# Optimization experiments

Measured on AMD Instinct MI355X. Metric: run time of the kernel, lower is better.

## Reference

```python
import jax, jax.numpy as jnp
import numpy as np

BITS = 8
EPS = 1e-5
NUM_HEADS = 16


def ste_round(x):
    # straight-through rounding (matches brevitas round STE)
    return x + jax.lax.stop_gradient(jnp.round(x) - x)


def _scale(stat, qmax):
    return jnp.maximum(stat, 1e-8) / qmax


def fq_act_signed(x, bits=BITS):
    # runtime max-abs per-tensor scale (approximates brevitas runtime percentile 99.999)
    qmax = 2 ** (bits - 1) - 1
    qmin = -(2 ** (bits - 1))
    s = _scale(jnp.max(jnp.abs(x)), qmax)
    return jnp.clip(ste_round(x / s), qmin, qmax) * s


def fq_act_unsigned(x, bits=BITS):
    qmax = 2 ** bits - 1
    s = _scale(jnp.max(x), qmax)
    return jnp.clip(ste_round(x / s), 0, qmax) * s


def fq_weight(w, bits=BITS):
    # NarrowIntQuant + MaxStatsScaling: symmetric narrow range [-qmax, qmax]
    qmax = 2 ** (bits - 1) - 1
    s = _scale(jnp.max(jnp.abs(w)), qmax)
    return jnp.clip(ste_round(w / s), -qmax, qmax) * s


def fq_bias(b, bits=BITS):
    qmax = 2 ** (bits - 1) - 1
    qmin = -(2 ** (bits - 1))
    s = _scale(jnp.max(jnp.abs(b)), qmax)
    return jnp.clip(ste_round(b / s), qmin, qmax) * s


def layernorm(x):
    # elementwise_affine=False
    m = jnp.mean(x, axis=-1, keepdims=True)
    v = jnp.mean((x - m) ** 2, axis=-1, keepdims=True)
    return (x - m) / jnp.sqrt(v + EPS)


def setup_inputs() -> dict:
    key = jax.random.key(0)
    ks = jax.random.split(key, 13)
    B, S, E, M = 4, 1024, 1024, 4096
    std = 0.02
    inp = {
        "x": jax.random.normal(ks[0], (B, S, E), jnp.float32),
        "Wq": jax.random.normal(ks[1], (E, E), jnp.float32) * std,
        "bq": jax.random.normal(ks[2], (E,), jnp.float32) * std,
        "Wk": jax.random.normal(ks[3], (E, E), jnp.float32) * std,
        "bk": jax.random.normal(ks[4], (E,), jnp.float32) * std,
        "Wv": jax.random.normal(ks[5], (E, E), jnp.float32) * std,
        "bv": jax.random.normal(ks[6], (E,), jnp.float32) * std,
        "Wo": jax.random.normal(ks[7], (E, E), jnp.float32) * std,
        "bo": jax.random.normal(ks[8], (E,), jnp.float32) * std,
        "W1": jax.random.normal(ks[9], (M, E), jnp.float32) * std,
        "b1": jax.random.normal(ks[10], (M,), jnp.float32) * std,
        "W2": jax.random.normal(ks[11], (E, M), jnp.float32) * std,
        "b2": jax.random.normal(ks[12], (E,), jnp.float32) * std,
    }
    return inp


def reference(x, Wq, bq, Wk, bk, Wv, bv, Wo, bo, W1, b1, W2, b2):
    B, S, E = x.shape
    H = NUM_HEADS
    D = E // H
    # causal additive mask [S, S]
    i = jnp.arange(S)
    mask = jnp.where(i[None, :] <= i[:, None], 0.0, -jnp.inf).astype(x.dtype)

    # sdp_input_quant (shared q=k=v input)
    q_in = fq_act_signed(x)

    # quantized in-proj (packed_in_proj=False -> separate q/k/v projections)
    Q = q_in @ fq_weight(Wq).T + fq_bias(bq)
    K = q_in @ fq_weight(Wk).T + fq_bias(bk)
    V = q_in @ fq_weight(Wv).T + fq_bias(bv)

    Qh = Q.reshape(B, S, H, D)
    Kh = K.reshape(B, S, H, D)
    Vh = V.reshape(B, S, H, D)

    qs = fq_act_signed(Qh / jnp.sqrt(jnp.asarray(D, x.dtype)))  # q_scaled_quant
    kq = fq_act_signed(Kh)  # k_transposed_quant (per-tensor -> transpose-invariant)
    vq = fq_act_signed(Vh)  # v_quant

    scores = jnp.einsum("bqhd,bkhd->bhqk", qs, kq) + mask  # [B,H,S,S]
    attn = fq_act_signed(jax.nn.softmax(scores, axis=-1))  # attn_output_weights_quant

    ctx = jnp.einsum("bhqk,bkhd->bqhd", attn, vq).reshape(B, S, E)
    ctx = fq_act_signed(ctx)  # out_proj_input_quant
    attn_out = ctx @ fq_weight(Wo).T + fq_bias(bo)

    # residual_sdp: QuantEltwiseAdd quantizes both inputs, then layer-norm
    x1 = layernorm(fq_act_signed(x) + fq_act_signed(attn_out))

    # MLP: QuantIdentity -> QuantLinear -> QuantReLU -> QuantLinear
    h = fq_act_signed(x1) @ fq_weight(W1).T + fq_bias(b1)
    h = fq_act_unsigned(jax.nn.relu(h))
    h = h @ fq_weight(W2).T + fq_bias(b2)

    out = layernorm(fq_act_signed(x1) + fq_act_signed(h))
    return out
```

## Files before the change

kernel.cpp:

```cpp
#include <hip/hip_runtime.h>
#include <stdint.h>
#include <stddef.h>


typedef unsigned short u16;
typedef __attribute__((ext_vector_type(4))) int   i32x4;
typedef __attribute__((ext_vector_type(4))) float f32x4;

#define DEV __device__ __forceinline__

DEV float bf2f(u16 u) { return __uint_as_float(((unsigned)u) << 16); }
DEV void atomicMaxF(float* p, float v) { atomicMax((unsigned*)p, __float_as_uint(v)); }
DEV float waveMax(float v) {
#pragma unroll
  for (int o = 32; o; o >>= 1) v = fmaxf(v, __shfl_xor(v, o, 64));
  return v;
}
DEV float waveSum(float v) {
#pragma unroll
  for (int o = 32; o; o >>= 1) v += __shfl_xor(v, o, 64);
  return v;
}
DEV int waveSumI(int v) {
#pragma unroll
  for (int o = 32; o; o >>= 1) v += __shfl_xor(v, o, 64);
  return v;
}
DEV void blockStatMax(float v, float* __restrict__ slot64, float* sred4, int flatBlk) {
  v = waveMax(v);
  const int tid = threadIdx.x;
  if ((tid & 63) == 0) sred4[tid >> 6] = v;
  __syncthreads();
  if (tid == 0) {
    float m = fmaxf(fmaxf(sred4[0], sred4[1]), fmaxf(sred4[2], sred4[3]));
    atomicMaxF(&slot64[flatBlk & 63], m);
  }
}
DEV float slotMax64(const float* __restrict__ s) {
  float m = 0.f;
#pragma unroll
  for (int i = 0; i < 64; ++i) m = fmaxf(m, s[i]);
  return m;
}
DEV f32x4 ld4(const void* p, int i4, int isf32) {
  if (isf32) return ((const f32x4*)p)[i4];
  ushort4 u = ((const ushort4*)p)[i4];
  return (f32x4){bf2f(u.x), bf2f(u.y), bf2f(u.z), bf2f(u.w)};
}
DEV void gll16(const void* g, void* l) {
  __builtin_amdgcn_global_load_lds((__attribute__((address_space(1))) void*)(g),
                                   (__attribute__((address_space(3))) void*)(l),
                                   16, 0, 0);
}
DEV unsigned ldsaddr(const void* p) {
  return (unsigned)(size_t)(__attribute__((address_space(3))) const void*)p;
}
DEV unsigned quadsel(unsigned a, unsigned b, unsigned c, unsigned d, int idx) {
  unsigned lo = (idx & 1) ? b : a;
  unsigned hi = (idx & 1) ? d : c;
  return (idx & 2) ? hi : lo;
}

__global__ void detect_f32(const u16* __restrict__ x, int* __restrict__ flag) {
  const int tid = threadIdx.x;
  int cnt = 0;
#pragma unroll
  for (int i = 0; i < 16; ++i) {
    u16 u = x[tid * 16 + i];
    if ((u & 0x7f80u) >= 0x4380u) ++cnt;
  }
  cnt = waveSumI(cnt);
  if (tid == 0) flag[0] = (cnt > 16) ? 1 : 0;
}

struct AJobs { const void* p[13]; int n4[13]; int bstart[14]; };

__global__ __launch_bounds__(256) void absmax_multi(AJobs J, float* __restrict__ M,
                                                    const int* __restrict__ flagp) {
  __shared__ float sred[4];
  const int isf32 = flagp[0];
  const int blk = blockIdx.x, tid = threadIdx.x;
  int j = 0;
  while (j < 12 && blk >= J.bstart[j + 1]) ++j;
  const int lb = blk - J.bstart[j];
  const int nb = J.bstart[j + 1] - J.bstart[j];
  float mx = 0.f;
  const void* p = J.p[j];
  for (int i = lb * 256 + tid; i < J.n4[j]; i += nb * 256) {
    f32x4 v = ld4(p, i, isf32);
    mx = fmaxf(mx, fmaxf(fmaxf(fabsf(v.x), fabsf(v.y)),
                         fmaxf(fabsf(v.z), fabsf(v.w))));
  }
  blockStatMax(mx, M + j * 64, sred, lb);
}

__global__ __launch_bounds__(256) void quant_in_signed(
    const void* __restrict__ in, int8_t* __restrict__ out,
    const float* __restrict__ mp, const int* __restrict__ flagp, int n4) {
  const int isf32 = flagp[0];
  const float s = fmaxf(slotMax64(mp), 1e-8f) / 127.0f;
  char4* op = (char4*)out;
  for (int i = blockIdx.x * 256 + threadIdx.x; i < n4; i += gridDim.x * 256) {
    f32x4 v = ld4(in, i, isf32);
    char4 q;
    q.x = (signed char)fminf(fmaxf(rintf(v.x / s), -128.f), 127.f);
    q.y = (signed char)fminf(fmaxf(rintf(v.y / s), -128.f), 127.f);
    q.z = (signed char)fminf(fmaxf(rintf(v.z / s), -128.f), 127.f);
    q.w = (signed char)fminf(fmaxf(rintf(v.w / s), -128.f), 127.f);
    op[i] = q;
  }
}

struct WJobs { const void* in[5]; int8_t* out[5]; int mslot[5]; int n4[5]; int bstart[6]; };

__global__ __launch_bounds__(256) void quant_w_multi(WJobs J, const float* __restrict__ M,
                                                     const int* __restrict__ flagp) {
  const int isf32 = flagp[0];
  const int blk = blockIdx.x, tid = threadIdx.x;
  int j = 0;
  while (j < 4 && blk >= J.bstart[j + 1]) ++j;
  const int lb = blk - J.bstart[j];
  const int nb = J.bstart[j + 1] - J.bstart[j];
  const float s = fmaxf(slotMax64(M + J.mslot[j] * 64), 1e-8f) / 127.0f;
  const void* p = J.in[j];
  char4* o = (char4*)J.out[j];
  for (int i = lb * 256 + tid; i < J.n4[j]; i += nb * 256) {
    f32x4 v = ld4(p, i, isf32);
    char4 q;
    q.x = (signed char)fminf(fmaxf(rintf(v.x / s), -127.f), 127.f);
    q.y = (signed char)fminf(fmaxf(rintf(v.y / s), -127.f), 127.f);
    q.z = (signed char)fminf(fmaxf(rintf(v.z / s), -127.f), 127.f);
    q.w = (signed char)fminf(fmaxf(rintf(v.w / s), -127.f), 127.f);
    o[i] = q;
  }
}

__global__ __launch_bounds__(256) void quant_w2_rs(
    const void* __restrict__ w2, int8_t* __restrict__ out,
    const float* __restrict__ mp, const int* __restrict__ flagp,
    int* __restrict__ rowsum) {
  const int isf32 = flagp[0];
  const int row = blockIdx.x, tid = threadIdx.x;
  const float s = fmaxf(slotMax64(mp), 1e-8f) / 127.0f;
  char4* op = (char4*)(out + (size_t)row * 4096);
  int sum = 0;
  for (int i = tid; i < 1024; i += 256) {
    f32x4 v = ld4(w2, row * 1024 + i, isf32);
    char4 q;
    q.x = (signed char)fminf(fmaxf(rintf(v.x / s), -127.f), 127.f);
    q.y = (signed char)fminf(fmaxf(rintf(v.y / s), -127.f), 127.f);
    q.z = (signed char)fminf(fmaxf(rintf(v.z / s), -127.f), 127.f);
    q.w = (signed char)fminf(fmaxf(rintf(v.w / s), -127.f), 127.f);
    op[i] = q;
    sum += (int)q.x + (int)q.y + (int)q.z + (int)q.w;
  }
  sum = waveSumI(sum);
  __shared__ int rs4[4];
  if ((tid & 63) == 0) rs4[tid >> 6] = sum;
  __syncthreads();
  if (tid == 0) rowsum[row] = rs4[0] + rs4[1] + rs4[2] + rs4[3];
}

struct BJobs { const void* in[6]; float* out[6]; int mslot[6]; int n4[6]; };

__global__ __launch_bounds__(256) void fq_bias_multi(BJobs J, const float* __restrict__ M,
                                                     const int* __restrict__ flagp) {
  const int isf32 = flagp[0];
  const int j = blockIdx.x;
  const float s = fmaxf(slotMax64(M + J.mslot[j] * 64), 1e-8f) / 127.0f;
  float* o = J.out[j];
  for (int i = threadIdx.x; i < J.n4[j]; i += 256) {
    f32x4 v = ld4(J.in[j], i, isf32);
    f32x4 r;
    r.x = fminf(fmaxf(rintf(v.x / s), -128.f), 127.f) * s;
    r.y = fminf(fmaxf(rintf(v.y / s), -128.f), 127.f) * s;
    r.z = fminf(fmaxf(rintf(v.z / s), -128.f), 127.f) * s;
    r.w = fminf(fmaxf(rintf(v.w / s), -128.f), 127.f) * s;
    *(f32x4*)(o + i * 4) = r;
  }
}

__global__ __launch_bounds__(256) void quant_f32_signed(
    const float* __restrict__ in, int8_t* __restrict__ out,
    const float* __restrict__ mp, float pre, int n4) {
  const float s = fmaxf(slotMax64(mp) * pre, 1e-8f) / 127.0f;
  const f32x4* ip = (const f32x4*)in;
  char4* op = (char4*)out;
  for (int i = blockIdx.x * 256 + threadIdx.x; i < n4; i += gridDim.x * 256) {
    f32x4 v = ip[i];
    char4 q;
    q.x = (signed char)fminf(fmaxf(rintf(v.x * pre / s), -128.f), 127.f);
    q.y = (signed char)fminf(fmaxf(rintf(v.y * pre / s), -128.f), 127.f);
    q.z = (signed char)fminf(fmaxf(rintf(v.z * pre / s), -128.f), 127.f);
    q.w = (signed char)fminf(fmaxf(rintf(v.w * pre / s), -128.f), 127.f);
    op[i] = q;
  }
}

__global__ __launch_bounds__(256) void quant_v_t(
    const float* __restrict__ V, int8_t* __restrict__ Vt,
    const float* __restrict__ mp) {
  __shared__ float tile[64][65];
  const int bh = blockIdx.x, st = blockIdx.y;
  const int b = bh >> 4, h = bh & 15;
  const int tid = threadIdx.x;
  const float s = fmaxf(slotMax64(mp), 1e-8f) / 127.0f;
  const int r = tid >> 2, c = (tid & 3) * 16;
  const float* src = V + ((size_t)(b * 1024 + st * 64 + r)) * 1024 + h * 64 + c;
#pragma unroll
  for (int g = 0; g < 4; ++g) {
    f32x4 v = *(const f32x4*)(src + g * 4);
    tile[r][c + g * 4 + 0] = v.x;
    tile[r][c + g * 4 + 1] = v.y;
    tile[r][c + g * 4 + 2] = v.z;
    tile[r][c + g * 4 + 3] = v.w;
  }
  __syncthreads();
  unsigned wds[4];
#pragma unroll
  for (int g = 0; g < 4; ++g) {
    unsigned wd = 0;
#pragma unroll
    for (int k = 0; k < 4; ++k) {
      float v = tile[c + g * 4 + k][r];
      int q = (int)fminf(fmaxf(rintf(v / s), -128.f), 127.f);
      wd |= ((unsigned)(unsigned char)(signed char)q) << (8 * k);
    }
    wds[g] = wd;
  }
  i32x4 ov = {(int)wds[0], (int)wds[1], (int)wds[2], (int)wds[3]};
  *(i32x4*)(Vt + ((size_t)((b * 16 + h) * 64 + r)) * 1024 + st * 64 + c) = ov;
}

__global__ __launch_bounds__(256) void gemm_i8(
    const int8_t* __restrict__ A, const int8_t* __restrict__ B,
    float* __restrict__ Cf, int8_t* __restrict__ Cq,
    const float* __restrict__ mA, float preA, float qmaxA,
    const float* __restrict__ mB,
    const float* __restrict__ bias, const int* __restrict__ extra,
    int relu, int mode, float* __restrict__ mOut, int K, int O) {
  __shared__ __align__(16) int8_t smem[4][12288];
  __shared__ float sred[4];
  const int tid = threadIdx.x;
  const int nb = blockIdx.x, ob = blockIdx.y;
  const int w = tid >> 6, lane = tid & 63, l15 = lane & 15, quad = lane >> 4;
  i32x4 acc[2][4];
#pragma unroll
  for (int i = 0; i < 2; ++i)
#pragma unroll
    for (int j = 0; j < 4; ++j) acc[i][j] = (i32x4){0, 0, 0, 0};
  const int r0 = tid >> 2, c0 = (tid & 3) * 16;
  const int8_t* Ab = A + (size_t)(nb * 128) * K;
  const int8_t* Bb = B + (size_t)(ob * 64) * K;
  const int nk = K >> 6;
  const int aoffl = (w * 32 + l15) * 64 + quad * 16;
  const int boffl = 8192 + l15 * 64 + quad * 16;
  for (int t = 0; t < 3 && t < nk; ++t) {
    const size_t kt0 = (size_t)t << 6;
    int8_t* d = smem[t];
    gll16(Ab + (size_t)r0 * K + kt0 + c0, d + tid * 16);
    gll16(Ab + (size_t)(r0 + 64) * K + kt0 + c0, d + 4096 + tid * 16);
    gll16(Bb + (size_t)r0 * K + kt0 + c0, d + 8192 + tid * 16);
  }
  for (int i = 0; i < nk; ++i) {
    const int infl = nk - 1 - i;
    if (infl >= 2)      asm volatile("s_waitcnt vmcnt(6)" ::: "memory");
    else if (infl == 1) asm volatile("s_waitcnt vmcnt(3)" ::: "memory");
    else                asm volatile("s_waitcnt vmcnt(0)" ::: "memory");
    asm volatile("s_barrier" ::: "memory");
    if (i + 3 < nk) {
      const size_t kt0 = (size_t)(i + 3) << 6;
      int8_t* d = smem[(i + 3) & 3];
      gll16(Ab + (size_t)r0 * K + kt0 + c0, d + tid * 16);
      gll16(Ab + (size_t)(r0 + 64) * K + kt0 + c0, d + 4096 + tid * 16);
      gll16(Bb + (size_t)r0 * K + kt0 + c0, d + 8192 + tid * 16);
    }
    const unsigned a_addr = ldsaddr(smem[i & 3] + aoffl);
    const unsigned b_addr = ldsaddr(smem[i & 3] + boffl);
    i32x4 af[2], bf[4];
    asm volatile("ds_read_b128 %0, %1 offset:0"    : "=v"(af[0]) : "v"(a_addr));
    asm volatile("ds_read_b128 %0, %1 offset:1024" : "=v"(af[1]) : "v"(a_addr));
    asm volatile("ds_read_b128 %0, %1 offset:0"    : "=v"(bf[0]) : "v"(b_addr));
    asm volatile("ds_read_b128 %0, %1 offset:1024" : "=v"(bf[1]) : "v"(b_addr));
    asm volatile("ds_read_b128 %0, %1 offset:2048" : "=v"(bf[2]) : "v"(b_addr));
    asm volatile("ds_read_b128 %0, %1 offset:3072" : "=v"(bf[3]) : "v"(b_addr));
    asm volatile("s_waitcnt lgkmcnt(0)" ::: "memory");
    __builtin_amdgcn_sched_barrier(0);
#pragma unroll
    for (int mt = 0; mt < 2; ++mt)
#pragma unroll
      for (int nt = 0; nt < 4; ++nt)
        acc[mt][nt] = __builtin_amdgcn_mfma_i32_16x16x64_i8(af[mt], bf[nt], acc[mt][nt], 0, 0, 0);
  }
  const float sA = fmaxf(slotMax64(mA) * preA, 1e-8f) / qmaxA;
  const float sB = fmaxf(slotMax64(mB), 1e-8f) / 127.0f;
  const float sAB = sA * sB;
  const float sq = (mode == 2) ? (fmaxf(slotMax64(mOut), 1e-8f) / 255.0f) : 1.0f;
  float lmax = 0.f;
#pragma unroll
  for (int mt = 0; mt < 2; ++mt) {
    const int n = nb * 128 + w * 32 + mt * 16 + quad * 4;
#pragma unroll
    for (int nt = 0; nt < 4; ++nt) {
      const int o = ob * 64 + nt * 16 + l15;
      const int ext = extra ? 128 * extra[o] : 0;
      const float bv = bias[o];
#pragma unroll
      for (int r = 0; r < 4; ++r) {
        float v = sAB * (float)(acc[mt][nt][r] + ext) + bv;
        if (relu) v = fmaxf(v, 0.f);
        if (mode == 0) Cf[(size_t)(n + r) * O + o] = v;
        else if (mode == 2) {
          int q = (int)fminf(fmaxf(rintf(v / sq), 0.f), 255.f) - 128;
          Cq[(size_t)(n + r) * O + o] = (int8_t)q;
        }
        lmax = fmaxf(lmax, fabsf(v));
      }
    }
  }
  if (mode != 2)
    blockStatMax(lmax, mOut, sred, nb + ob * gridDim.x);
}

__global__ __launch_bounds__(256, 4) void attn_fused(
    const int8_t* __restrict__ Qq, const int8_t* __restrict__ Kq,
    const int8_t* __restrict__ Vt, float* __restrict__ ctx,
    const float* __restrict__ M, float* __restrict__ mOut) {
  __shared__ __align__(16) int8_t qtile[4096];
  __shared__ __align__(16) int8_t ktile[4][4096];
  __shared__ __align__(16) int8_t vtile[4][4096];
  __shared__ float sred[4];
  const int tid = threadIdx.x, bid = blockIdx.x;
  const int pidx = bid & 7, rh = (bid >> 3) & 1, h = (bid >> 4) & 15, b = bid >> 8;
  const int qthi = 15 - pidx, qtlo = pidx, ktmax = qthi;
  const int w = tid >> 6, lane = tid & 63, l15 = lane & 15, quad = lane >> 4;
  const int wqt = (w < 2) ? qthi : qtlo;
  const int wrow0 = rh * 32 + (w & 1) * 16;
  const float sqs = fmaxf(slotMax64(M + 13 * 64) * 0.125f, 1e-8f) / 127.0f;
  const float sk = fmaxf(slotMax64(M + 14 * 64), 1e-8f) / 127.0f;
  const float sv = fmaxf(slotMax64(M + 15 * 64), 1e-8f) / 127.0f;
  const float sqk = sqs * sk;
  const float s_attn = 1.0f / 127.0f;
  const int r0 = tid >> 2, c0 = (tid & 3) * 16;
  const int8_t* Kbase = Kq + (size_t)(b * 1024) * 1024 + h * 64 + c0;
  const int8_t* Vbase = Vt + (size_t)((b * 16 + h) * 64 + r0) * 1024 + c0;
  const unsigned fragoff = (unsigned)(l15 * 64 + quad * 16);

  {
    const int qt_s = (r0 < 32) ? qthi : qtlo;
    const int qrow_g = qt_s * 64 + rh * 32 + (r0 & 31);
    gll16(Qq + ((size_t)(b * 1024 + qrow_g)) * 1024 + h * 64 + c0, qtile + tid * 16);
  }
#pragma unroll
  for (int t = 0; t < 3; ++t)
    gll16(Kbase + (size_t)(t * 64 + r0) * 1024, ktile[t] + tid * 16);
  asm volatile("s_waitcnt vmcnt(3)" ::: "memory");
  asm volatile("s_barrier" ::: "memory");
  i32x4 aq;
  {
    const unsigned qa = ldsaddr(qtile) + (unsigned)((w * 16 + l15) * 64 + quad * 16);
    asm volatile("ds_read_b128 %0, %1 offset:0" : "=v"(aq) : "v"(qa));
    asm volatile("s_waitcnt lgkmcnt(0)" ::: "memory");
  }
  const int qrow = wqt * 64 + wrow0 + l15;

  float m_l = -1e30f, l_l = 0.f;
  for (int kt = 0; kt <= ktmax; ++kt) {
    if (kt + 2 <= ktmax)      asm volatile("s_waitcnt vmcnt(2)" ::: "memory");
    else if (kt + 1 <= ktmax) asm volatile("s_waitcnt vmcnt(1)" ::: "memory");
    else                      asm volatile("s_waitcnt vmcnt(0)" ::: "memory");
    asm volatile("s_barrier" ::: "memory");
    if (kt + 3 <= ktmax)
      gll16(Kbase + (size_t)((kt + 3) * 64 + r0) * 1024, ktile[(kt + 3) & 3] + tid * 16);
    if (kt <= wqt) {
      const unsigned ka = ldsaddr(ktile[kt & 3]) + fragoff;
      i32x4 bk[4];
      asm volatile("ds_read_b128 %0, %1 offset:0"    : "=v"(bk[0]) : "v"(ka));
      asm volatile("ds_read_b128 %0, %1 offset:1024" : "=v"(bk[1]) : "v"(ka));
      asm volatile("ds_read_b128 %0, %1 offset:2048" : "=v"(bk[2]) : "v"(ka));
      asm volatile("ds_read_b128 %0, %1 offset:3072" : "=v"(bk[3]) : "v"(ka));
      asm volatile("s_waitcnt lgkmcnt(0)" ::: "memory");
      __builtin_amdgcn_sched_barrier(0);
      const int kc0 = kt * 64 + quad * 4;
      float sc[4][4];
#pragma unroll
      for (int nt = 0; nt < 4; ++nt) {
        i32x4 z = {0, 0, 0, 0};
        i32x4 d = __builtin_amdgcn_mfma_i32_16x16x64_i8(bk[nt], aq, z, 0, 0, 0);
        if (kt == wqt) {
#pragma unroll
          for (int r = 0; r < 4; ++r)
            sc[nt][r] = (kc0 + nt * 16 + r <= qrow) ? sqk * (float)d[r] : -1e30f;
        } else {
#pragma unroll
          for (int r = 0; r < 4; ++r) sc[nt][r] = sqk * (float)d[r];
        }
      }
      float vm = sc[0][0];
#pragma unroll
      for (int nt = 0; nt < 4; ++nt)
#pragma unroll
        for (int r = 0; r < 4; ++r) vm = fmaxf(vm, sc[nt][r]);
      const float mn = fmaxf(m_l, vm);
      float sum = 0.f;
#pragma unroll
      for (int nt = 0; nt < 4; ++nt)
#pragma unroll
        for (int r = 0; r < 4; ++r) sum += __expf(sc[nt][r] - mn);
      l_l = l_l * __expf(m_l - mn) + sum;
      m_l = mn;
    }
  }
#pragma unroll
  for (int off = 16; off <= 32; off <<= 1) {
    float om = __shfl_xor(m_l, off, 64);
    float ol = __shfl_xor(l_l, off, 64);
    float mn = fmaxf(m_l, om);
    l_l = l_l * __expf(m_l - mn) + ol * __expf(om - mn);
    m_l = mn;
  }
  const float rl127 = 127.0f / l_l;

  __syncthreads();
#pragma unroll
  for (int t = 0; t < 3; ++t) {
    gll16(Kbase + (size_t)(t * 64 + r0) * 1024, ktile[t] + tid * 16);
    gll16(Vbase + t * 64, vtile[t] + tid * 16);
  }
  i32x4 cacc[4] = {{0, 0, 0, 0}, {0, 0, 0, 0}, {0, 0, 0, 0}, {0, 0, 0, 0}};
  for (int kt = 0; kt <= ktmax; ++kt) {
    if (kt + 2 <= ktmax)      asm volatile("s_waitcnt vmcnt(4)" ::: "memory");
    else if (kt + 1 <= ktmax) asm volatile("s_waitcnt vmcnt(2)" ::: "memory");
    else                      asm volatile("s_waitcnt vmcnt(0)" ::: "memory");
    asm volatile("s_barrier" ::: "memory");
    if (kt + 3 <= ktmax) {
      gll16(Kbase + (size_t)((kt + 3) * 64 + r0) * 1024, ktile[(kt + 3) & 3] + tid * 16);
      gll16(Vbase + (kt + 3) * 64, vtile[(kt + 3) & 3] + tid * 16);
    }
    if (kt <= wqt) {
      const unsigned ka = ldsaddr(ktile[kt & 3]) + fragoff;
      const unsigned va = ldsaddr(vtile[kt & 3]) + fragoff;
      i32x4 bk[4], bv[4];
      asm volatile("ds_read_b128 %0, %1 offset:0"    : "=v"(bk[0]) : "v"(ka));
      asm volatile("ds_read_b128 %0, %1 offset:1024" : "=v"(bk[1]) : "v"(ka));
      asm volatile("ds_read_b128 %0, %1 offset:2048" : "=v"(bk[2]) : "v"(ka));
      asm volatile("ds_read_b128 %0, %1 offset:3072" : "=v"(bk[3]) : "v"(ka));
      asm volatile("ds_read_b128 %0, %1 offset:0"    : "=v"(bv[0]) : "v"(va));
      asm volatile("ds_read_b128 %0, %1 offset:1024" : "=v"(bv[1]) : "v"(va));
      asm volatile("ds_read_b128 %0, %1 offset:2048" : "=v"(bv[2]) : "v"(va));
      asm volatile("ds_read_b128 %0, %1 offset:3072" : "=v"(bv[3]) : "v"(va));
      asm volatile("s_waitcnt lgkmcnt(0)" ::: "memory");
      __builtin_amdgcn_sched_barrier(0);
      const int kc0 = kt * 64 + quad * 4;
      unsigned Dw[4];
#pragma unroll
      for (int nt = 0; nt < 4; ++nt) {
        i32x4 z = {0, 0, 0, 0};
        i32x4 d = __builtin_amdgcn_mfma_i32_16x16x64_i8(bk[nt], aq, z, 0, 0, 0);
        unsigned wd = 0;
        if (kt == wqt) {
#pragma unroll
          for (int r = 0; r < 4; ++r) {
            float e = (kc0 + nt * 16 + r <= qrow)
                          ? __expf(sqk * (float)d[r] - m_l) * rl127 : 0.f;
            wd |= ((unsigned)(int)rintf(e)) << (8 * r);
          }
        } else {
#pragma unroll
          for (int r = 0; r < 4; ++r) {
            float e = __expf(sqk * (float)d[r] - m_l) * rl127;
            wd |= ((unsigned)(int)rintf(e)) << (8 * r);
          }
        }
        Dw[nt] = wd;
      }
      unsigned selfv = quadsel(Dw[0], Dw[1], Dw[2], Dw[3], quad);
      unsigned rv1 = (unsigned)__shfl_xor(
          (int)quadsel(Dw[0], Dw[1], Dw[2], Dw[3], quad ^ 1), 16, 64);
      unsigned rv2 = (unsigned)__shfl_xor(
          (int)quadsel(Dw[0], Dw[1], Dw[2], Dw[3], quad ^ 2), 32, 64);
      unsigned rv3 = (unsigned)__shfl_xor(
          (int)quadsel(Dw[0], Dw[1], Dw[2], Dw[3], quad ^ 3), 48, 64);
      i32x4 pf;
#pragma unroll
      for (int j = 0; j < 4; ++j) {
        const int t = j ^ quad;
        pf[j] = (int)((t == 0) ? selfv : (t == 1) ? rv1 : (t == 2) ? rv2 : rv3);
      }
#pragma unroll
      for (int nt = 0; nt < 4; ++nt)
        cacc[nt] = __builtin_amdgcn_mfma_i32_16x16x64_i8(pf, bv[nt], cacc[nt], 0, 0, 0);
    }
  }
  const float sc2 = s_attn * sv;
  float lmax = 0.f;
  const int orow0 = wqt * 64 + wrow0 + quad * 4;
#pragma unroll
  for (int nt = 0; nt < 4; ++nt) {
    const int d = nt * 16 + l15;
#pragma unroll
    for (int r = 0; r < 4; ++r) {
      float v = sc2 * (float)cacc[nt][r];
      ctx[((size_t)(b * 1024 + orow0 + r)) * 1024 + h * 64 + d] = v;
      lmax = fmaxf(lmax, fabsf(v));
    }
  }
  blockStatMax(lmax, mOut, sred, bid);
}

__global__ __launch_bounds__(256) void ln_res(
    const int8_t* __restrict__ xq, const float* __restrict__ mx,
    const float* __restrict__ ao, const float* __restrict__ ma,
    float* __restrict__ x1, float* __restrict__ mOut) {
  __shared__ float red[8];
  __shared__ float sred[4];
  const int row = blockIdx.x, tid = threadIdx.x;
  const float sx = fmaxf(slotMax64(mx), 1e-8f) / 127.0f;
  const float sa = fmaxf(slotMax64(ma), 1e-8f) / 127.0f;
  char4 xv = *(const char4*)(xq + (size_t)row * 1024 + tid * 4);
  f32x4 av = *(const f32x4*)(ao + (size_t)row * 1024 + tid * 4);
  float t[4];
  t[0] = (float)xv.x * sx + fminf(fmaxf(rintf(av.x / sa), -128.f), 127.f) * sa;
  t[1] = (float)xv.y * sx + fminf(fmaxf(rintf(av.y / sa), -128.f), 127.f) * sa;
  t[2] = (float)xv.z * sx + fminf(fmaxf(rintf(av.z / sa), -128.f), 127.f) * sa;
  t[3] = (float)xv.w * sx + fminf(fmaxf(rintf(av.w / sa), -128.f), 127.f) * sa;
  float s = waveSum(t[0] + t[1] + t[2] + t[3]);
  if ((tid & 63) == 0) red[tid >> 6] = s;
  __syncthreads();
  const float mean = (red[0] + red[1] + red[2] + red[3]) * (1.0f / 1024.0f);
  float vs = 0.f;
#pragma unroll
  for (int i = 0; i < 4; ++i) { float d = t[i] - mean; vs += d * d; }
  vs = waveSum(vs);
  if ((tid & 63) == 0) red[4 + (tid >> 6)] = vs;
  __syncthreads();
  const float var = (red[4] + red[5] + red[6] + red[7]) * (1.0f / 1024.0f);
  const float rs = sqrtf(var + 1e-5f);
  f32x4 o;
  o.x = (t[0] - mean) / rs;
  o.y = (t[1] - mean) / rs;
  o.z = (t[2] - mean) / rs;
  o.w = (t[3] - mean) / rs;
  *(f32x4*)(x1 + (size_t)row * 1024 + tid * 4) = o;
  float lmax = fmaxf(fmaxf(fabsf(o.x), fabsf(o.y)), fmaxf(fabsf(o.z), fabsf(o.w)));
  blockStatMax(lmax, mOut, sred, row);
}

__global__ __launch_bounds__(256) void ln_final(
    const int8_t* __restrict__ x1q, const float* __restrict__ mx1,
    const float* __restrict__ h2, const float* __restrict__ mh2,
    float* __restrict__ out) {
  __shared__ float red[8];
  const int row = blockIdx.x, tid = threadIdx.x;
  const float s1 = fmaxf(slotMax64(mx1), 1e-8f) / 127.0f;
  const float s2 = fmaxf(slotMax64(mh2), 1e-8f) / 127.0f;
  char4 xv = *(const char4*)(x1q + (size_t)row * 1024 + tid * 4);
  f32x4 hv = *(const f32x4*)(h2 + (size_t)row * 1024 + tid * 4);
  float t[4];
  t[0] = (float)xv.x * s1 + fminf(fmaxf(rintf(hv.x / s2), -128.f), 127.f) * s2;
  t[1] = (float)xv.y * s1 + fminf(fmaxf(rintf(hv.y / s2), -128.f), 127.f) * s2;
  t[2] = (float)xv.z * s1 + fminf(fmaxf(rintf(hv.z / s2), -128.f), 127.f) * s2;
  t[3] = (float)xv.w * s1 + fminf(fmaxf(rintf(hv.w / s2), -128.f), 127.f) * s2;
  float s = waveSum(t[0] + t[1] + t[2] + t[3]);
  if ((tid & 63) == 0) red[tid >> 6] = s;
  __syncthreads();
  const float mean = (red[0] + red[1] + red[2] + red[3]) * (1.0f / 1024.0f);
  float vs = 0.f;
#pragma unroll
  for (int i = 0; i < 4; ++i) { float d = t[i] - mean; vs += d * d; }
  vs = waveSum(vs);
  if ((tid & 63) == 0) red[4 + (tid >> 6)] = vs;
  __syncthreads();
  const float var = (red[4] + red[5] + red[6] + red[7]) * (1.0f / 1024.0f);
  const float rs = sqrtf(var + 1e-5f);
  f32x4 o;
  o.x = (t[0] - mean) / rs;
  o.y = (t[1] - mean) / rs;
  o.z = (t[2] - mean) / rs;
  o.w = (t[3] - mean) / rs;
  *(f32x4*)(out + (size_t)row * 1024 + tid * 4) = o;
}

static constexpr size_t MB = 1u << 20;
static constexpr size_t OFF_M     = 0;
static constexpr size_t OFF_FLAG  = 6400;
static constexpr size_t OFF_BIASQ = 8192;
static constexpr size_t OFF_BIASK = OFF_BIASQ + 4096;
static constexpr size_t OFF_BIASV = OFF_BIASK + 4096;
static constexpr size_t OFF_BIASO = OFF_BIASV + 4096;
static constexpr size_t OFF_BIAS1 = OFF_BIASO + 4096;
static constexpr size_t OFF_BIAS2 = OFF_BIAS1 + 16384;
static constexpr size_t OFF_RS    = OFF_BIAS2 + 4096;
static constexpr size_t OFF_XQ    = 65536;
static constexpr size_t OFF_WQQ   = OFF_XQ  + 4 * MB;
static constexpr size_t OFF_WKQ   = OFF_WQQ + 1 * MB;
static constexpr size_t OFF_WVQ   = OFF_WKQ + 1 * MB;
static constexpr size_t OFF_WOQ   = OFF_WVQ + 1 * MB;
static constexpr size_t OFF_W1Q   = OFF_WOQ + 1 * MB;
static constexpr size_t OFF_W2Q   = OFF_W1Q + 4 * MB;
static constexpr size_t OFF_X1Q   = OFF_W2Q + 4 * MB;
static constexpr size_t OFF_A1    = OFF_X1Q + 4 * MB;
static constexpr size_t OFF_A2    = OFF_A1 + 16 * MB;

extern "C" void kernel_launch(void* const* d_in, const int* in_sizes, int n_in,
                              void* d_out, int out_size, void* d_ws, size_t ws_size,
                              hipStream_t stream) {
  (void)n_in; (void)out_size; (void)ws_size;
  char* ws = (char*)d_ws;
  float* M = (float*)(ws + OFF_M);
  int* FLAG = (int*)(ws + OFF_FLAG);
  float* BIASQ = (float*)(ws + OFF_BIASQ);
  float* BIASK = (float*)(ws + OFF_BIASK);
  float* BIASV = (float*)(ws + OFF_BIASV);
  float* BIASO = (float*)(ws + OFF_BIASO);
  float* BIAS1 = (float*)(ws + OFF_BIAS1);
  float* BIAS2 = (float*)(ws + OFF_BIAS2);
  int* RS = (int*)(ws + OFF_RS);
  int8_t* XQ  = (int8_t*)(ws + OFF_XQ);
  int8_t* WQQ = (int8_t*)(ws + OFF_WQQ);
  int8_t* WKQ = (int8_t*)(ws + OFF_WKQ);
  int8_t* WVQ = (int8_t*)(ws + OFF_WVQ);
  int8_t* WOQ = (int8_t*)(ws + OFF_WOQ);
  int8_t* W1Q = (int8_t*)(ws + OFF_W1Q);
  int8_t* W2Q = (int8_t*)(ws + OFF_W2Q);
  int8_t* X1Q = (int8_t*)(ws + OFF_X1Q);
  int8_t* QQ   = (int8_t*)(ws + OFF_A1);
  int8_t* KQQ  = (int8_t*)(ws + OFF_A1 + 4 * MB);
  int8_t* VT   = (int8_t*)(ws + OFF_A1 + 8 * MB);
  int8_t* CTXQ = (int8_t*)(ws + OFF_A1 + 12 * MB);
  float*  X1F  = (float*)(ws + OFF_A1);
  int8_t* HQ   = (int8_t*)(ws + OFF_A1);
  float* FBUF = (float*)(ws + OFF_A2);

  hipMemsetAsync(M, 0, 8192, stream);
  detect_f32<<<1, 64, 0, stream>>>((const u16*)d_in[0], FLAG);

  AJobs aj;
  const int ablk[13] = {512, 128, 1, 128, 1, 128, 1, 128, 1, 512, 2, 512, 1};
  int bs = 0;
  for (int i = 0; i < 13; ++i) {
    aj.p[i] = d_in[i];
    aj.n4[i] = in_sizes[i] / 4;
    aj.bstart[i] = bs;
    bs += ablk[i];
  }
  aj.bstart[13] = bs;
  absmax_multi<<<bs, 256, 0, stream>>>(aj, M, FLAG);

  quant_in_signed<<<1024, 256, 0, stream>>>(d_in[0], XQ, M + 0 * 64, FLAG, in_sizes[0] / 4);

  WJobs wj;
  const int widx[5] = {1, 3, 5, 7, 9};
  int8_t* wout[5] = {WQQ, WKQ, WVQ, WOQ, W1Q};
  const int wblk[5] = {128, 128, 128, 128, 512};
  int wb = 0;
  for (int j = 0; j < 5; ++j) {
    wj.in[j] = d_in[widx[j]];
    wj.out[j] = wout[j];
    wj.mslot[j] = widx[j];
    wj.n4[j] = in_sizes[widx[j]] / 4;
    wj.bstart[j] = wb;
    wb += wblk[j];
  }
  wj.bstart[5] = wb;
  quant_w_multi<<<wb, 256, 0, stream>>>(wj, M, FLAG);
  quant_w2_rs<<<1024, 256, 0, stream>>>(d_in[11], W2Q, M + 11 * 64, FLAG, RS);

  BJobs bj;
  const int bidx[6] = {2, 4, 6, 8, 10, 12};
  float* bout[6] = {BIASQ, BIASK, BIASV, BIASO, BIAS1, BIAS2};
  for (int j = 0; j < 6; ++j) {
    bj.in[j] = d_in[bidx[j]];
    bj.out[j] = bout[j];
    bj.mslot[j] = bidx[j];
    bj.n4[j] = in_sizes[bidx[j]] / 4;
  }
  fq_bias_multi<<<6, 256, 0, stream>>>(bj, M, FLAG);

  gemm_i8<<<dim3(32, 16), 256, 0, stream>>>(XQ, WQQ, FBUF, nullptr, M + 0 * 64, 1.f, 127.f, M + 1 * 64, BIASQ, nullptr, 0, 0, M + 13 * 64, 1024, 1024);
  quant_f32_signed<<<2048, 256, 0, stream>>>(FBUF, QQ, M + 13 * 64, 0.125f, 1024 * 1024);
  gemm_i8<<<dim3(32, 16), 256, 0, stream>>>(XQ, WKQ, FBUF, nullptr, M + 0 * 64, 1.f, 127.f, M + 3 * 64, BIASK, nullptr, 0, 0, M + 14 * 64, 1024, 1024);
  quant_f32_signed<<<2048, 256, 0, stream>>>(FBUF, KQQ, M + 14 * 64, 1.0f, 1024 * 1024);
  gemm_i8<<<dim3(32, 16), 256, 0, stream>>>(XQ, WVQ, FBUF, nullptr, M + 0 * 64, 1.f, 127.f, M + 5 * 64, BIASV, nullptr, 0, 0, M + 15 * 64, 1024, 1024);
  quant_v_t<<<dim3(64, 16), 256, 0, stream>>>(FBUF, VT, M + 15 * 64);

  attn_fused<<<1024, 256, 0, stream>>>(QQ, KQQ, VT, FBUF, M, M + 16 * 64);
  quant_f32_signed<<<2048, 256, 0, stream>>>(FBUF, CTXQ, M + 16 * 64, 1.0f, 1024 * 1024);

  gemm_i8<<<dim3(32, 16), 256, 0, stream>>>(CTXQ, WOQ, FBUF, nullptr, M + 16 * 64, 1.f, 127.f, M + 7 * 64, BIASO, nullptr, 0, 0, M + 17 * 64, 1024, 1024);

  ln_res<<<4096, 256, 0, stream>>>(XQ, M + 0 * 64, FBUF, M + 17 * 64, X1F, M + 18 * 64);
  quant_f32_signed<<<2048, 256, 0, stream>>>(X1F, X1Q, M + 18 * 64, 1.0f, 1024 * 1024);

  gemm_i8<<<dim3(32, 64), 256, 0, stream>>>(X1Q, W1Q, nullptr, nullptr, M + 18 * 64, 1.f, 127.f, M + 9 * 64, BIAS1, nullptr, 1, 1, M + 19 * 64, 1024, 4096);
  gemm_i8<<<dim3(32, 64), 256, 0, stream>>>(X1Q, W1Q, nullptr, HQ,      M + 18 * 64, 1.f, 127.f, M + 9 * 64, BIAS1, nullptr, 1, 2, M + 19 * 64, 1024, 4096);

  gemm_i8<<<dim3(32, 16), 256, 0, stream>>>(HQ, W2Q, FBUF, nullptr, M + 19 * 64, 1.f, 255.f, M + 11 * 64, BIAS2, RS, 0, 0, M + 20 * 64, 4096, 1024);

  ln_final<<<4096, 256, 0, stream>>>(X1Q, M + 18 * 64, FBUF, M + 20 * 64, (float*)d_out);
}
```

Baseline: 428.7 us.

## Swizzle LDS tiles in int8 GEMM/attention and store MLP hidden once

Applies an XOR swizzle to the 16-byte column slot of LDS tiles in the int8 GEMM and fused attention kernels, both on the global-to-LDS writes and on the fragment reads, to reduce LDS bank conflicts. When the workspace is large enough, the first MLP GEMM also runs only once: it writes fp32 pre-activations to a new buffer, and a separate kernel quantizes them to offset uint8. This replaces the earlier pattern of running the GEMM twice, once for the max and once for quantization. The trade is roughly 64 MB of extra fp32 write and read traffic in exchange for skipping a full recompute of the 4096-wide GEMM.

```diff
diff --git a/kernel.cpp b/kernel.cpp
--- a/kernel.cpp
+++ b/kernel.cpp
@@ -197,6 +197,23 @@
   }
 }
 
+__global__ __launch_bounds__(256) void quant_f32_u8(
+    const float* __restrict__ in, int8_t* __restrict__ out,
+    const float* __restrict__ mp, int n4) {
+  const float s = fmaxf(slotMax64(mp), 1e-8f) / 255.0f;
+  const f32x4* ip = (const f32x4*)in;
+  char4* op = (char4*)out;
+  for (int i = blockIdx.x * 256 + threadIdx.x; i < n4; i += gridDim.x * 256) {
+    f32x4 v = ip[i];
+    char4 q;
+    q.x = (signed char)((int)fminf(fmaxf(rintf(v.x / s), 0.f), 255.f) - 128);
+    q.y = (signed char)((int)fminf(fmaxf(rintf(v.y / s), 0.f), 255.f) - 128);
+    q.z = (signed char)((int)fminf(fmaxf(rintf(v.z / s), 0.f), 255.f) - 128);
+    q.w = (signed char)((int)fminf(fmaxf(rintf(v.w / s), 0.f), 255.f) - 128);
+    op[i] = q;
+  }
+}
+
 __global__ __launch_bounds__(256) void quant_v_t(
     const float* __restrict__ V, int8_t* __restrict__ Vt,
     const float* __restrict__ mp) {
@@ -249,12 +266,14 @@
   for (int i = 0; i < 2; ++i)
 #pragma unroll
     for (int j = 0; j < 4; ++j) acc[i][j] = (i32x4){0, 0, 0, 0};
-  const int r0 = tid >> 2, c0 = (tid & 3) * 16;
+  const int r0 = tid >> 2;
+  const int c0 = (((tid & 3) ^ ((tid >> 2) & 3)) * 16);
   const int8_t* Ab = A + (size_t)(nb * 128) * K;
   const int8_t* Bb = B + (size_t)(ob * 64) * K;
   const int nk = K >> 6;
-  const int aoffl = (w * 32 + l15) * 64 + quad * 16;
-  const int boffl = 8192 + l15 * 64 + quad * 16;
+  const int slot = (quad ^ (l15 & 3)) * 16;
+  const int aoffl = (w * 32 + l15) * 64 + slot;
+  const int boffl = 8192 + l15 * 64 + slot;
   for (int t = 0; t < 3 && t < nk; ++t) {
     const size_t kt0 = (size_t)t << 6;
     int8_t* d = smem[t];
@@ -341,10 +360,11 @@
   const float sv = fmaxf(slotMax64(M + 15 * 64), 1e-8f) / 127.0f;
   const float sqk = sqs * sk;
   const float s_attn = 1.0f / 127.0f;
-  const int r0 = tid >> 2, c0 = (tid & 3) * 16;
+  const int r0 = tid >> 2;
+  const int c0 = (((tid & 3) ^ ((tid >> 2) & 3)) * 16);
   const int8_t* Kbase = Kq + (size_t)(b * 1024) * 1024 + h * 64 + c0;
   const int8_t* Vbase = Vt + (size_t)((b * 16 + h) * 64 + r0) * 1024 + c0;
-  const unsigned fragoff = (unsigned)(l15 * 64 + quad * 16);
+  const unsigned fragoff = (unsigned)(l15 * 64 + (quad ^ (l15 & 3)) * 16);
 
   {
     const int qt_s = (r0 < 32) ? qthi : qtlo;
@@ -358,7 +378,8 @@
   asm volatile("s_barrier" ::: "memory");
   i32x4 aq;
   {
-    const unsigned qa = ldsaddr(qtile) + (unsigned)((w * 16 + l15) * 64 + quad * 16);
+    const unsigned qa = ldsaddr(qtile) +
+        (unsigned)((w * 16 + l15) * 64 + (quad ^ (l15 & 3)) * 16);
     asm volatile("ds_read_b128 %0, %1 offset:0" : "=v"(aq) : "v"(qa));
     asm volatile("s_waitcnt lgkmcnt(0)" ::: "memory");
   }
@@ -601,11 +622,12 @@
 static constexpr size_t OFF_X1Q   = OFF_W2Q + 4 * MB;
 static constexpr size_t OFF_A1    = OFF_X1Q + 4 * MB;
 static constexpr size_t OFF_A2    = OFF_A1 + 16 * MB;
+static constexpr size_t OFF_HF    = OFF_A2 + 16 * MB;
 
 extern "C" void kernel_launch(void* const* d_in, const int* in_sizes, int n_in,
                               void* d_out, int out_size, void* d_ws, size_t ws_size,
                               hipStream_t stream) {
-  (void)n_in; (void)out_size; (void)ws_size;
+  (void)n_in; (void)out_size;
   char* ws = (char*)d_ws;
   float* M = (float*)(ws + OFF_M);
   int* FLAG = (int*)(ws + OFF_FLAG);
@@ -631,6 +653,7 @@
   float*  X1F  = (float*)(ws + OFF_A1);
   int8_t* HQ   = (int8_t*)(ws + OFF_A1);
   float* FBUF = (float*)(ws + OFF_A2);
+  const bool bigws = ws_size >= OFF_HF + 64 * MB;
 
   hipMemsetAsync(M, 0, 8192, stream);
   detect_f32<<<1, 64, 0, stream>>>((const u16*)d_in[0], FLAG);
@@ -692,8 +715,14 @@
   ln_res<<<4096, 256, 0, stream>>>(XQ, M + 0 * 64, FBUF, M + 17 * 64, X1F, M + 18 * 64);
   quant_f32_signed<<<2048, 256, 0, stream>>>(X1F, X1Q, M + 18 * 64, 1.0f, 1024 * 1024);
 
-  gemm_i8<<<dim3(32, 64), 256, 0, stream>>>(X1Q, W1Q, nullptr, nullptr, M + 18 * 64, 1.f, 127.f, M + 9 * 64, BIAS1, nullptr, 1, 1, M + 19 * 64, 1024, 4096);
-  gemm_i8<<<dim3(32, 64), 256, 0, stream>>>(X1Q, W1Q, nullptr, HQ,      M + 18 * 64, 1.f, 127.f, M + 9 * 64, BIAS1, nullptr, 1, 2, M + 19 * 64, 1024, 4096);
+  if (bigws) {
+    float* HF = (float*)(ws + OFF_HF);
+    gemm_i8<<<dim3(32, 64), 256, 0, stream>>>(X1Q, W1Q, HF, nullptr, M + 18 * 64, 1.f, 127.f, M + 9 * 64, BIAS1, nullptr, 1, 0, M + 19 * 64, 1024, 4096);
+    quant_f32_u8<<<2048, 256, 0, stream>>>(HF, HQ, M + 19 * 64, 4096 * 1024);
+  } else {
+    gemm_i8<<<dim3(32, 64), 256, 0, stream>>>(X1Q, W1Q, nullptr, nullptr, M + 18 * 64, 1.f, 127.f, M + 9 * 64, BIAS1, nullptr, 1, 1, M + 19 * 64, 1024, 4096);
+    gemm_i8<<<dim3(32, 64), 256, 0, stream>>>(X1Q, W1Q, nullptr, HQ,      M + 18 * 64, 1.f, 127.f, M + 9 * 64, BIAS1, nullptr, 1, 2, M + 19 * 64, 1024, 4096);
+  }
 
   gemm_i8<<<dim3(32, 16), 256, 0, stream>>>(HQ, W2Q, FBUF, nullptr, M + 19 * 64, 1.f, 255.f, M + 11 * 64, BIAS2, RS, 0, 0, M + 20 * 64, 4096, 1024);
 
```

Result: faster. 409.8 us (-4.4%).
